# Kernel tuning notes

Measured on AMD Instinct MI355X. Metric: run time of the kernel, lower is better.

The kernel has to match this reference:

```python
import jax, jax.numpy as jnp
import numpy as np

N = 100000
E_ADJ = 800000
E_RAY = 800000
IN_DIM = 2
HID = 64
HEADS = 2
NEG_SLOPE = 0.2  # PyG GATv2Conv default


def setup_inputs() -> dict:
    key = jax.random.key(0)
    ks = jax.random.split(key, 16)
    s = 0.1
    p = lambda k, shape: (jax.random.normal(k, shape, jnp.float32) * s)
    inp = {
        "x": jax.random.normal(ks[0], (N, IN_DIM), jnp.float32),
        "edge_adj": jax.random.randint(ks[1], (2, E_ADJ), 0, N, jnp.int32),
        "edge_ray": jax.random.randint(ks[2], (2, E_RAY), 0, N, jnp.int32),
        # layer 1 params, stacked over the 2 relation types [adjacent, ray]
        "l1_Wl": p(ks[3], (2, IN_DIM, HEADS * HID)),
        "l1_bl": jnp.zeros((2, HEADS * HID), jnp.float32),
        "l1_Wr": p(ks[4], (2, IN_DIM, HEADS * HID)),
        "l1_br": jnp.zeros((2, HEADS * HID), jnp.float32),
        "l1_att": p(ks[5], (2, HEADS, HID)),
        "l1_bias": jnp.zeros((2, HID), jnp.float32),
        # layer 2 params
        "l2_Wl": p(ks[6], (2, HID, HEADS * HID)),
        "l2_bl": jnp.zeros((2, HEADS * HID), jnp.float32),
        "l2_Wr": p(ks[7], (2, HID, HEADS * HID)),
        "l2_br": jnp.zeros((2, HEADS * HID), jnp.float32),
        "l2_att": p(ks[8], (2, HEADS, HID)),
        "l2_bias": jnp.zeros((2, HID), jnp.float32),
    }
    return inp


def _gatv2(x, src, dst, Wl, bl, Wr, br, att, bias):
    # GATv2Conv, concat=False, add_self_loops=False (PyG semantics)
    n = x.shape[0]
    H, C = att.shape
    xl = (x @ Wl + bl).reshape(n, H, C)  # source transform
    xr = (x @ Wr + br).reshape(n, H, C)  # target transform
    e = jax.nn.leaky_relu(xl[src] + xr[dst], NEG_SLOPE)  # [E,H,C]
    score = jnp.einsum('ehc,hc->eh', e, att)             # [E,H]
    # segment softmax over incoming edges per destination (per head)
    m = jax.ops.segment_max(score, dst, num_segments=n)  # only gathered at non-empty segs
    ex = jnp.exp(score - m[dst])
    denom = jax.ops.segment_sum(ex, dst, num_segments=n)
    alpha = ex / (denom[dst] + 1e-16)                    # [E,H]
    out = jax.ops.segment_sum(xl[src] * alpha[:, :, None], dst, num_segments=n)  # [N,H,C]
    return out.mean(axis=1) + bias                       # concat=False -> head mean


def _hetero_layer(x, ea, er, Wl, bl, Wr, br, att, bias):
    o_adj = _gatv2(x, ea[0], ea[1], Wl[0], bl[0], Wr[0], br[0], att[0], bias[0])
    o_ray = _gatv2(x, er[0], er[1], Wl[1], bl[1], Wr[1], br[1], att[1], bias[1])
    return 0.5 * (o_adj + o_ray)  # HeteroConv aggr='mean' over 2 relations


def reference(x, edge_adj, edge_ray,
              l1_Wl, l1_bl, l1_Wr, l1_br, l1_att, l1_bias,
              l2_Wl, l2_bl, l2_Wr, l2_br, l2_att, l2_bias):
    h = _hetero_layer(x, edge_adj, edge_ray, l1_Wl, l1_bl, l1_Wr, l1_br, l1_att, l1_bias)
    h = jax.nn.relu(h)
    out = _hetero_layer(h, edge_adj, edge_ray, l2_Wl, l2_bl, l2_Wr, l2_br, l2_att, l2_bias)
    return out
```

## Files before the change

### kernel.cpp

```cpp
#include <hip/hip_runtime.h>
#include <hip/hip_bf16.h>

typedef __hip_bfloat16 bf16;
typedef unsigned int uint;
typedef unsigned short ushort;
typedef __attribute__((ext_vector_type(8))) short short8;
typedef __attribute__((ext_vector_type(4))) float floatx4;

#define N_NODES 100000
#define N_PAD   100096
#define E_EDGES 800000
#define NBLK    98
#define NSLICE  8
#define SLICE_N 12512
#define SLICE_BLOCKS 512

static __device__ __forceinline__ uint packbf(float a, float b) {
  bf16 x = __float2bfloat16(a), y = __float2bfloat16(b);
  ushort ux = *reinterpret_cast<ushort*>(&x);
  ushort uy = *reinterpret_cast<ushort*>(&y);
  return (uint)ux | ((uint)uy << 16);
}
static __device__ __forceinline__ float lo16(uint u) { return __uint_as_float(u << 16); }
static __device__ __forceinline__ float hi16(uint u) { return __uint_as_float(u & 0xffff0000u); }

__global__ void hist_sliced_k(const int* __restrict__ dst0, const int* __restrict__ dst1,
                              int* dg0, int* dg1) {
  int slice = blockIdx.x & (NSLICE - 1);
  int blk = blockIdx.x >> 3;
  int lo = slice * SLICE_N, hi = lo + SLICE_N;
  for (int i = blk * 256 + threadIdx.x; i < E_EDGES; i += SLICE_BLOCKS * 256) {
    int d0 = __builtin_nontemporal_load(dst0 + i);
    if (d0 >= lo && d0 < hi) atomicAdd(&dg0[d0], 1);
    int d1 = __builtin_nontemporal_load(dst1 + i);
    if (d1 >= lo && d1 < hi) atomicAdd(&dg1[d1], 1);
  }
}

__global__ void scat_sliced_k(const int* __restrict__ src0, const int* __restrict__ dst0,
                              const int* __restrict__ src1, const int* __restrict__ dst1,
                              int* fi0, int* fi1, int2* csd0, int2* csd1) {
  int slice = blockIdx.x & (NSLICE - 1);
  int blk = blockIdx.x >> 3;
  int lo = slice * SLICE_N, hi = lo + SLICE_N;
  for (int i = blk * 256 + threadIdx.x; i < E_EDGES; i += SLICE_BLOCKS * 256) {
    int d0 = __builtin_nontemporal_load(dst0 + i);
    if (d0 >= lo && d0 < hi) {
      int s = __builtin_nontemporal_load(src0 + i);
      int p = atomicAdd(&fi0[d0], 1);
      csd0[p] = make_int2(s, d0);
    }
    int d1 = __builtin_nontemporal_load(dst1 + i);
    if (d1 >= lo && d1 < hi) {
      int s = __builtin_nontemporal_load(src1 + i);
      int p = atomicAdd(&fi1[d1], 1);
      csd1[p] = make_int2(s, d1);
    }
  }
}

__global__ void scan_blk_k(const int* __restrict__ deg0, const int* __restrict__ deg1,
                           int* rp0, int* rp1, int* bsum) {
  __shared__ int s[1024];
  int r = blockIdx.y;
  const int* deg = r ? deg1 : deg0;
  int* rp = r ? rp1 : rp0;
  int i = blockIdx.x * 1024 + threadIdx.x;
  int v = (i < N_NODES) ? deg[i] : 0;
  s[threadIdx.x] = v;
  __syncthreads();
  for (int off = 1; off < 1024; off <<= 1) {
    int t = (threadIdx.x >= off) ? s[threadIdx.x - off] : 0;
    __syncthreads();
    s[threadIdx.x] += t;
    __syncthreads();
  }
  if (i < N_NODES) rp[i] = s[threadIdx.x] - v;
  if (threadIdx.x == 1023) bsum[r * NBLK + blockIdx.x] = s[1023];
}

__global__ void scan_top_k(int* bsum, int* rp0, int* rp1) {
  __shared__ int s[128];
  int r = blockIdx.x;
  int v = (threadIdx.x < NBLK) ? bsum[r * NBLK + threadIdx.x] : 0;
  s[threadIdx.x] = v;
  __syncthreads();
  for (int off = 1; off < 128; off <<= 1) {
    int t = (threadIdx.x >= off) ? s[threadIdx.x - off] : 0;
    __syncthreads();
    s[threadIdx.x] += t;
    __syncthreads();
  }
  if (threadIdx.x < NBLK) bsum[r * NBLK + threadIdx.x] = s[threadIdx.x] - v;
  if (threadIdx.x == 127) (r ? rp1 : rp0)[N_NODES] = s[127];
}

__global__ void scan_add_k(const int* __restrict__ bsum,
                           int* rp0, int* rp1, int* fi0, int* fi1) {
  int r = blockIdx.y;
  int i = blockIdx.x * 1024 + threadIdx.x;
  if (i >= N_NODES) return;
  int* rp = r ? rp1 : rp0;
  int* fi = r ? fi1 : fi0;
  int val = rp[i] + bsum[r * NBLK + blockIdx.x];
  rp[i] = val;
  fi[i] = val;
}

__global__ void wprep_k(const float* __restrict__ Wl, const float* __restrict__ Wr,
                        short* __restrict__ WT,
                        const float* __restrict__ l1Wl, const float* __restrict__ l1bl,
                        const float* __restrict__ l1Wr, const float* __restrict__ l1br,
                        const float* __restrict__ l1att, float* __restrict__ L1C) {
  if (blockIdx.x == 128) {
    int t = threadIdx.x;
    if (t < 20) {
      int rel = t / 10, rem = t % 10, h = rem / 5, v = rem % 5;
      const float* a = l1att + rel * 128 + h * 64;
      float sum = 0.f;
      for (int c = 0; c < 64; ++c) {
        int cc = h * 64 + c;
        float val;
        if (v == 0)      val = l1bl[rel * 128 + cc] + l1br[rel * 128 + cc];
        else if (v == 1) val = l1Wr[rel * 256 + cc];
        else if (v == 2) val = l1Wr[rel * 256 + 128 + cc];
        else if (v == 3) val = l1Wl[rel * 256 + cc];
        else             val = l1Wl[rel * 256 + 128 + cc];
        sum += a[c] * val;
      }
      L1C[t] = sum;
    }
    return;
  }
  int id2 = blockIdx.x * 256 + threadIdx.x;
  int rel = id2 >> 14;
  int id = id2 & 16383;
  int c = id >> 6, k = id & 63;
  const float* W = (c < 128) ? (Wl + rel * 8192) : (Wr + rel * 8192);
  int cc = c & 127;
  bf16 b = __float2bfloat16(W[k * 128 + cc]);
  WT[rel * 16384 + c * 64 + k] = *reinterpret_cast<short*>(&b);
}

__global__ __launch_bounds__(256) void l1score_k(
    const int2* __restrict__ csd0, const int2* __restrict__ csd1,
    const float* __restrict__ x,
    const float* __restrict__ Wl, const float* __restrict__ bl,
    const float* __restrict__ Wr, const float* __restrict__ br,
    const float* __restrict__ att, const float* __restrict__ l1c,
    float4* __restrict__ EX4) {
  __shared__ float sC[32 * 24];
  int rel = blockIdx.y;
  const int2* csd = rel ? csd1 : csd0;
  const float* Wl_r = Wl + rel * 256;
  const float* Wr_r = Wr + rel * 256;
  const float* bl_r = bl + rel * 128;
  const float* br_r = br + rel * 128;
  const float* att_r = att + rel * 128;
  int t = threadIdx.x;
  if (t < 128) {
    int c = t, ch = c >> 2, o = c & 3;
    sC[ch * 24 + 0 + o]  = bl_r[c] + br_r[c];
    sC[ch * 24 + 4 + o]  = Wr_r[c];
    sC[ch * 24 + 8 + o]  = Wr_r[128 + c];
    sC[ch * 24 + 12 + o] = Wl_r[c];
    sC[ch * 24 + 16 + o] = Wl_r[128 + c];
    sC[ch * 24 + 20 + o] = att_r[c];
  }
  const float* C = l1c + rel * 10;
  float q00 = C[0], qv00 = C[1], qv10 = C[2], qw00 = C[3], qw10 = C[4];
  float q01 = C[5], qv01 = C[6], qv11 = C[7], qw01 = C[8], qw11 = C[9];
  __syncthreads();
  int i = blockIdx.x * 256 + t;
  int2 sd = csd[i];
  int s = sd.x, d = sd.y;
  float2 xs = *(const float2*)(x + 2 * s);
  float2 xd = *(const float2*)(x + 2 * d);
  float t0a = 0.f, t0b = 0.f, t1a = 0.f, t1b = 0.f;
#pragma unroll
  for (int ch = 0; ch < 32; ++ch) {
    const float4* cp = (const float4*)(sC + ch * 24);
    float4 bb = cp[0], v0 = cp[1], v1 = cp[2], w0 = cp[3], w1 = cp[4], aa = cp[5];
    float e0 = bb.x + xd.x * v0.x + xd.y * v1.x + xs.x * w0.x + xs.y * w1.x;
    float e1 = bb.y + xd.x * v0.y + xd.y * v1.y + xs.x * w0.y + xs.y * w1.y;
    float e2 = bb.z + xd.x * v0.z + xd.y * v1.z + xs.x * w0.z + xs.y * w1.z;
    float e3 = bb.w + xd.x * v0.w + xd.y * v1.w + xs.x * w0.w + xs.y * w1.w;
    if (ch < 16) {
      t0a = fmaf(aa.x, fabsf(e0), t0a); t0b = fmaf(aa.y, fabsf(e1), t0b);
      t0a = fmaf(aa.z, fabsf(e2), t0a); t0b = fmaf(aa.w, fabsf(e3), t0b);
    } else {
      t1a = fmaf(aa.x, fabsf(e0), t1a); t1b = fmaf(aa.y, fabsf(e1), t1b);
      t1a = fmaf(aa.z, fabsf(e2), t1a); t1b = fmaf(aa.w, fabsf(e3), t1b);
    }
  }
  float T0 = t0a + t0b, T1 = t1a + t1b;
  float lin0 = q00 + xd.x * qv00 + xd.y * qv10 + xs.x * qw00 + xs.y * qw10;
  float lin1 = q01 + xd.x * qv01 + xd.y * qv11 + xs.x * qw01 + xs.y * qw11;
  float p0 = fmaf(0.4f, T0, 0.6f * lin0);
  float p1 = fmaf(0.4f, T1, 0.6f * lin1);
  EX4[(size_t)rel * E_EDGES + i] = make_float4(__expf(p0), __expf(p1), xs.x, xs.y);
}

__global__ __launch_bounds__(256) void l1agg_k(
    const int* __restrict__ rp0, const int* __restrict__ rp1,
    const float4* __restrict__ EX4, float* __restrict__ NA) {
  int g = (blockIdx.x * 256 + threadIdx.x) >> 2;
  int k = threadIdx.x & 3;
  if (g >= N_NODES) return;
  float p0 = 0.f, p1 = 0.f, p2 = 0.f, p3 = 0.f, p4 = 0.f, p5 = 0.f;
  float p6 = 0.f, p7 = 0.f, p8 = 0.f, p9 = 0.f, p10 = 0.f, p11 = 0.f;
  {
    int beg = rp0[g], end = rp0[g + 1];
    for (int j = beg + k; j < end; j += 4) {
      float4 e = EX4[j];
      p0 += e.x; p1 = fmaf(e.x, e.z, p1); p2 = fmaf(e.x, e.w, p2);
      p3 += e.y; p4 = fmaf(e.y, e.z, p4); p5 = fmaf(e.y, e.w, p5);
    }
  }
  {
    const float4* E1 = EX4 + E_EDGES;
    int beg = rp1[g], end = rp1[g + 1];
    for (int j = beg + k; j < end; j += 4) {
      float4 e = E1[j];
      p6 += e.x; p7 = fmaf(e.x, e.z, p7); p8 = fmaf(e.x, e.w, p8);
      p9 += e.y; p10 = fmaf(e.y, e.z, p10); p11 = fmaf(e.y, e.w, p11);
    }
  }
#define RED4(v) v += __shfl_xor(v, 1); v += __shfl_xor(v, 2);
  RED4(p0) RED4(p1) RED4(p2) RED4(p3) RED4(p4) RED4(p5)
  RED4(p6) RED4(p7) RED4(p8) RED4(p9) RED4(p10) RED4(p11)
#undef RED4
  float* na = NA + (size_t)g * 16;
  if (k == 0)      *(float4*)(na)     = make_float4(p0, p1, p2, p3);
  else if (k == 1) *(float4*)(na + 4) = make_float4(p4, p5, p6, p7);
  else if (k == 2) *(float4*)(na + 8) = make_float4(p8, p9, p10, p11);
}

__global__ __launch_bounds__(256) void l1finish_k(
    const float* __restrict__ NA,
    const float* __restrict__ Wl, const float* __restrict__ bl,
    const float* __restrict__ bias, uint2* __restrict__ HB2) {
  int idx = blockIdx.x * 256 + threadIdx.x;
  int d = idx >> 4, l = idx & 15;
  int c0 = 4 * l;
  const float* na = NA + (size_t)d * 16;
  float out0 = 0.f, out1 = 0.f, out2 = 0.f, out3 = 0.f;
#pragma unroll
  for (int r = 0; r < 2; ++r) {
    float a0c = 0.f, a1c = 0.f, a2c = 0.f, a3c = 0.f;
#pragma unroll
    for (int h = 0; h < 2; ++h) {
      float den = na[r * 6 + h * 3 + 0];
      float A0  = na[r * 6 + h * 3 + 1];
      float A1  = na[r * 6 + h * 3 + 2];
      float inv = 1.f / (den + 1e-16f);
      float a0 = A0 * inv, a1 = A1 * inv, S = den * inv;
      float4 W0 = *(const float4*)(Wl + r * 256 + h * 64 + c0);
      float4 W1 = *(const float4*)(Wl + r * 256 + 128 + h * 64 + c0);
      float4 B  = *(const float4*)(bl + r * 128 + h * 64 + c0);
      a0c += a0 * W0.x + a1 * W1.x + S * B.x;
      a1c += a0 * W0.y + a1 * W1.y + S * B.y;
      a2c += a0 * W0.z + a1 * W1.z + S * B.z;
      a3c += a0 * W0.w + a1 * W1.w + S * B.w;
    }
    float4 bi = *(const float4*)(bias + r * 64 + c0);
    out0 += 0.5f * a0c + bi.x;
    out1 += 0.5f * a1c + bi.y;
    out2 += 0.5f * a2c + bi.z;
    out3 += 0.5f * a3c + bi.w;
  }
  out0 = fmaxf(0.5f * out0, 0.f); out1 = fmaxf(0.5f * out1, 0.f);
  out2 = fmaxf(0.5f * out2, 0.f); out3 = fmaxf(0.5f * out3, 0.f);
  HB2[(size_t)d * 16 + l] = make_uint2(packbf(out0, out1), packbf(out2, out3));
}

__global__ __launch_bounds__(256) void mfma_t_k(const bf16* __restrict__ HB,
                                                const short* __restrict__ WTb,
                                                const float* __restrict__ blb,
                                                const float* __restrict__ brb,
                                                bf16* __restrict__ XL0,
                                                bf16* __restrict__ XR0,
                                                bf16* __restrict__ XL1,
                                                bf16* __restrict__ XR1) {
  __shared__ short sW[256 * 72];
  int rel = blockIdx.z;
  const short* WT = WTb + rel * 16384;
  const float* bl = blb + rel * 128;
  const float* br = brb + rel * 128;
  bf16* XLp = rel ? XL1 : XL0;
  bf16* XRp = rel ? XR1 : XR0;
  int t = threadIdx.x;
#pragma unroll
  for (int i = 0; i < 8; ++i) {
    int chunk = t + i * 256;
    int c = chunk >> 3, off = (chunk & 7) * 8;
    *(short8*)(&sW[c * 72 + off]) = *(const short8*)(WT + chunk * 8);
  }
  __syncthreads();
  int wave = t >> 6, lane = t & 63;
  int q = lane >> 4, m = lane & 15;
  int rowbase = blockIdx.x * 128 + wave * 32;
  short8 afr[2][2];
#pragma unroll
  for (int rt = 0; rt < 2; ++rt)
#pragma unroll
    for (int kh = 0; kh < 2; ++kh) {
      size_t row = (size_t)(rowbase + rt * 16 + m);
      afr[rt][kh] = *(const short8*)((const short*)HB + row * 64 + kh * 32 + q * 8);
    }
  for (int ct = 0; ct < 16; ++ct) {
    int col = ct * 16 + m;
    short8 b0 = *(const short8*)(&sW[col * 72 + q * 8]);
    short8 b1 = *(const short8*)(&sW[col * 72 + 32 + q * 8]);
    float bias = (col < 128) ? bl[col] : br[col - 128];
    bf16* X = (col < 128) ? XLp : XRp;
    int c128 = col & 127;
#pragma unroll
    for (int rt = 0; rt < 2; ++rt) {
      floatx4 acc = {0.f, 0.f, 0.f, 0.f};
      acc = __builtin_amdgcn_mfma_f32_16x16x32_bf16(afr[rt][0], b0, acc, 0, 0, 0);
      acc = __builtin_amdgcn_mfma_f32_16x16x32_bf16(afr[rt][1], b1, acc, 0, 0, 0);
      int r0 = rowbase + rt * 16 + q * 4;
#pragma unroll
      for (int i2 = 0; i2 < 4; ++i2) {
        int row = r0 + i2;
        if (row < N_NODES)
          X[(size_t)row * 128 + c128] = __float2bfloat16(acc[i2] + bias);
      }
    }
  }
}

struct EdgeAcc { float a0, a1, a2, a3, den; };

static __device__ __forceinline__ void edge_step(
    uint2 u, float xr0, float xr1, float xr2, float xr3,
    float at0, float at1, float at2, float at3, EdgeAcc& A) {
  float x0 = lo16(u.x), x1 = hi16(u.x), x2 = lo16(u.y), x3 = hi16(u.y);
  float e0 = x0 + xr0; e0 = e0 > 0.f ? e0 : 0.2f * e0;
  float e1 = x1 + xr1; e1 = e1 > 0.f ? e1 : 0.2f * e1;
  float e2 = x2 + xr2; e2 = e2 > 0.f ? e2 : 0.2f * e2;
  float e3 = x3 + xr3; e3 = e3 > 0.f ? e3 : 0.2f * e3;
  float p = e0 * at0 + e1 * at1 + e2 * at2 + e3 * at3;
  p += __shfl_xor(p, 1);
  p += __shfl_xor(p, 2);
  p += __shfl_xor(p, 4);
  p += __shfl_xor(p, 8);
  float ex = __expf(p);
  A.den += ex;
  A.a0 += ex * x0; A.a1 += ex * x1; A.a2 += ex * x2; A.a3 += ex * x3;
}

__global__ __launch_bounds__(256) void aggh_k(
    const int* __restrict__ rp, const int2* __restrict__ csd,
    const bf16* __restrict__ XL, const bf16* __restrict__ XR,
    const float* __restrict__ att, const float* __restrict__ bias,
    float* __restrict__ accum, float* __restrict__ outf, int phase) {
  int d = (blockIdx.x * 256 + threadIdx.x) >> 6;
  int lane = threadIdx.x & 63;
  if (d >= N_NODES) return;
  int half = lane >> 5;
  int l = lane & 31;
  const float* at = att + 4 * l;
  float at0 = at[0], at1 = at[1], at2 = at[2], at3 = at[3];
  uint2 ur = *(const uint2*)(XR + (size_t)d * 128 + 4 * l);
  float xr0 = lo16(ur.x), xr1 = hi16(ur.x), xr2 = lo16(ur.y), xr3 = hi16(ur.y);
  EdgeAcc A = {0.f, 0.f, 0.f, 0.f, 0.f};
  int beg = rp[d], end = rp[d + 1];
  int j = beg + half;
  for (; j + 2 < end; j += 4) {
    int sA = csd[j].x, sB = csd[j + 2].x;
    uint2 uA = *(const uint2*)(XL + (size_t)sA * 128 + 4 * l);
    uint2 uB = *(const uint2*)(XL + (size_t)sB * 128 + 4 * l);
    edge_step(uA, xr0, xr1, xr2, xr3, at0, at1, at2, at3, A);
    edge_step(uB, xr0, xr1, xr2, xr3, at0, at1, at2, at3, A);
  }
  for (; j < end; j += 2) {
    int s = csd[j].x;
    uint2 u = *(const uint2*)(XL + (size_t)s * 128 + 4 * l);
    edge_step(u, xr0, xr1, xr2, xr3, at0, at1, at2, at3, A);
  }
  A.den += __shfl_xor(A.den, 32);
  A.a0 += __shfl_xor(A.a0, 32);
  A.a1 += __shfl_xor(A.a1, 32);
  A.a2 += __shfl_xor(A.a2, 32);
  A.a3 += __shfl_xor(A.a3, 32);
  float inv = 1.f / (A.den + 1e-16f);
  A.a0 *= inv; A.a1 *= inv; A.a2 *= inv; A.a3 *= inv;
  float o0 = 0.5f * (A.a0 + __shfl_xor(A.a0, 16));
  float o1 = 0.5f * (A.a1 + __shfl_xor(A.a1, 16));
  float o2 = 0.5f * (A.a2 + __shfl_xor(A.a2, 16));
  float o3 = 0.5f * (A.a3 + __shfl_xor(A.a3, 16));
  if (lane >= 16) return;
  int c0 = 4 * lane;
  o0 += bias[c0]; o1 += bias[c0 + 1]; o2 += bias[c0 + 2]; o3 += bias[c0 + 3];
  size_t oi = (size_t)d * 64 + c0;
  if (phase == 0) {
    *(float4*)(accum + oi) = make_float4(o0, o1, o2, o3);
  } else {
    float4 pa = *(const float4*)(accum + oi);
    float v0 = 0.5f * (pa.x + o0);
    float v1 = 0.5f * (pa.y + o1);
    float v2 = 0.5f * (pa.z + o2);
    float v3 = 0.5f * (pa.w + o3);
    *(float4*)(outf + oi) = make_float4(v0, v1, v2, v3);
  }
}

extern "C" void kernel_launch(void* const* d_in, const int* in_sizes, int n_in,
                              void* d_out, int out_size, void* d_ws, size_t ws_size,
                              hipStream_t stream) {
  const float* x       = (const float*)d_in[0];
  const int*   e_adj   = (const int*)d_in[1];
  const int*   e_ray   = (const int*)d_in[2];
  const float* l1_Wl   = (const float*)d_in[3];
  const float* l1_bl   = (const float*)d_in[4];
  const float* l1_Wr   = (const float*)d_in[5];
  const float* l1_br   = (const float*)d_in[6];
  const float* l1_att  = (const float*)d_in[7];
  const float* l1_bias = (const float*)d_in[8];
  const float* l2_Wl   = (const float*)d_in[9];
  const float* l2_bl   = (const float*)d_in[10];
  const float* l2_Wr   = (const float*)d_in[11];
  const float* l2_br   = (const float*)d_in[12];
  const float* l2_att  = (const float*)d_in[13];
  const float* l2_bias = (const float*)d_in[14];
  float* out = (float*)d_out;

  char* w = (char*)d_ws;
  size_t off = 0;
  auto alloc = [&](size_t bytes) -> char* {
    char* p = w + off;
    off += (bytes + 255) & ~(size_t)255;
    return p;
  };
  bf16* XL0  = (bf16*)alloc((size_t)N_PAD * 128 * 2);
  bf16* XR0  = (bf16*)alloc((size_t)N_PAD * 128 * 2);
  bf16* XL1  = (bf16*)alloc((size_t)N_PAD * 128 * 2);
  bf16* XR1  = (bf16*)alloc((size_t)N_PAD * 128 * 2);
  bf16* HB   = (bf16*)alloc((size_t)N_PAD * 64 * 2);
  short* WT  = (short*)alloc(2 * 16384 * 2);
  int* RP0   = (int*)alloc((size_t)(N_NODES + 1) * 4);
  int* RP1   = (int*)alloc((size_t)(N_NODES + 1) * 4);
  int* FI0   = (int*)alloc((size_t)N_NODES * 4);
  int* FI1   = (int*)alloc((size_t)N_NODES * 4);
  int2* CSD0 = (int2*)alloc((size_t)E_EDGES * 8);
  int2* CSD1 = (int2*)alloc((size_t)E_EDGES * 8);
  int* DG0   = (int*)alloc((size_t)N_NODES * 4);
  int* DG1   = (int*)alloc((size_t)N_NODES * 4);
  int* BSUM  = (int*)alloc(2 * NBLK * 4);
  float* L1C = (float*)alloc(20 * 4);
  float* ACC = out;

  float4* EX4 = (float4*)XL0;
  float* NA   = (float*)((char*)XL0 + 25600000);

  const int* src_adj = e_adj;
  const int* dst_adj = e_adj + E_EDGES;
  const int* src_ray = e_ray;
  const int* dst_ray = e_ray + E_EDGES;

  const int WNB = (N_NODES * 64) / 256;
  const int MB  = N_PAD / 128;
  const int SB  = SLICE_BLOCKS * NSLICE;

  size_t dgspan = (size_t)((char*)DG1 - (char*)DG0) + (size_t)N_NODES * 4;
  hipMemsetAsync(DG0, 0, dgspan, stream);
  hist_sliced_k<<<SB, 256, 0, stream>>>(dst_adj, dst_ray, DG0, DG1);
  scan_blk_k<<<dim3(NBLK, 2), 1024, 0, stream>>>(DG0, DG1, RP0, RP1, BSUM);
  scan_top_k<<<2, 128, 0, stream>>>(BSUM, RP0, RP1);
  scan_add_k<<<dim3(NBLK, 2), 1024, 0, stream>>>(BSUM, RP0, RP1, FI0, FI1);
  scat_sliced_k<<<SB, 256, 0, stream>>>(src_adj, dst_adj, src_ray, dst_ray,
                                        FI0, FI1, CSD0, CSD1);
  wprep_k<<<129, 256, 0, stream>>>(l2_Wl, l2_Wr, WT,
                                   l1_Wl, l1_bl, l1_Wr, l1_br, l1_att, L1C);

  l1score_k<<<dim3(E_EDGES / 256, 2), 256, 0, stream>>>(
      CSD0, CSD1, x, l1_Wl, l1_bl, l1_Wr, l1_br, l1_att, L1C, EX4);
  l1agg_k<<<(N_NODES * 4 + 255) / 256, 256, 0, stream>>>(RP0, RP1, EX4, NA);
  l1finish_k<<<(N_NODES * 16) / 256, 256, 0, stream>>>(NA, l1_Wl, l1_bl, l1_bias,
                                                       (uint2*)HB);

  mfma_t_k<<<dim3(MB, 1, 2), 256, 0, stream>>>(HB, WT, l2_bl, l2_br,
                                               XL0, XR0, XL1, XR1);
  aggh_k<<<WNB, 256, 0, stream>>>(RP0, CSD0, XL0, XR0, l2_att, l2_bias,
                                  ACC, nullptr, 0);
  aggh_k<<<WNB, 256, 0, stream>>>(RP1, CSD1, XL1, XR1, l2_att + 128, l2_bias + 64,
                                  ACC, out, 1);
}
```

Measured before the change: 492.7 us.

## Partition edges by destination slice once before the CSR histogram and scatter

```diff
diff --git a/kernel.cpp b/kernel.cpp
--- a/kernel.cpp
+++ b/kernel.cpp
@@ -13,7 +13,8 @@
 #define NBLK    98
 #define NSLICE  8
 #define SLICE_N 12512
-#define SLICE_BLOCKS 512
+#define PCAP    384
+#define PBLK    512
 
 static __device__ __forceinline__ uint packbf(float a, float b) {
   bf16 x = __float2bfloat16(a), y = __float2bfloat16(b);
@@ -24,38 +25,119 @@
 static __device__ __forceinline__ float lo16(uint u) { return __uint_as_float(u << 16); }
 static __device__ __forceinline__ float hi16(uint u) { return __uint_as_float(u & 0xffff0000u); }
 
-__global__ void hist_sliced_k(const int* __restrict__ dst0, const int* __restrict__ dst1,
-                              int* dg0, int* dg1) {
-  int slice = blockIdx.x & (NSLICE - 1);
-  int blk = blockIdx.x >> 3;
-  int lo = slice * SLICE_N, hi = lo + SLICE_N;
-  for (int i = blk * 256 + threadIdx.x; i < E_EDGES; i += SLICE_BLOCKS * 256) {
-    int d0 = __builtin_nontemporal_load(dst0 + i);
-    if (d0 >= lo && d0 < hi) atomicAdd(&dg0[d0], 1);
-    int d1 = __builtin_nontemporal_load(dst1 + i);
-    if (d1 >= lo && d1 < hi) atomicAdd(&dg1[d1], 1);
-  }
-}
-
-__global__ void scat_sliced_k(const int* __restrict__ src0, const int* __restrict__ dst0,
-                              const int* __restrict__ src1, const int* __restrict__ dst1,
-                              int* fi0, int* fi1, int2* csd0, int2* csd1) {
-  int slice = blockIdx.x & (NSLICE - 1);
-  int blk = blockIdx.x >> 3;
-  int lo = slice * SLICE_N, hi = lo + SLICE_N;
-  for (int i = blk * 256 + threadIdx.x; i < E_EDGES; i += SLICE_BLOCKS * 256) {
-    int d0 = __builtin_nontemporal_load(dst0 + i);
-    if (d0 >= lo && d0 < hi) {
-      int s = __builtin_nontemporal_load(src0 + i);
-      int p = atomicAdd(&fi0[d0], 1);
-      csd0[p] = make_int2(s, d0);
-    }
-    int d1 = __builtin_nontemporal_load(dst1 + i);
-    if (d1 >= lo && d1 < hi) {
-      int s = __builtin_nontemporal_load(src1 + i);
-      int p = atomicAdd(&fi1[d1], 1);
-      csd1[p] = make_int2(s, d1);
-    }
+__global__ __launch_bounds__(256) void bhist_k(const int* __restrict__ dst0,
+                                               const int* __restrict__ dst1,
+                                               int* __restrict__ bcnt) {
+  __shared__ int h[16];
+  int t = threadIdx.x;
+  if (t < 16) h[t] = 0;
+  __syncthreads();
+  for (int i = blockIdx.x * 256 + t; i < E_EDGES; i += 1024 * 256) {
+    atomicAdd(&h[dst0[i] / SLICE_N], 1);
+    atomicAdd(&h[8 + dst1[i] / SLICE_N], 1);
+  }
+  __syncthreads();
+  if (t < 16 && h[t]) atomicAdd(&bcnt[t], h[t]);
+}
+
+__global__ void bscan_k(const int* __restrict__ bcnt, int* __restrict__ bbase,
+                        int* __restrict__ gtail) {
+  if (threadIdx.x == 0) {
+    for (int r = 0; r < 2; ++r) {
+      int run = 0;
+      for (int b = 0; b < 8; ++b) {
+        int idx = r * 8 + b;
+        bbase[idx] = run;
+        gtail[idx] = run;
+        run += bcnt[idx];
+      }
+    }
+  }
+}
+
+__global__ __launch_bounds__(256) void part_k(
+    const int* __restrict__ src0, const int* __restrict__ dst0,
+    const int* __restrict__ src1, const int* __restrict__ dst1,
+    int* __restrict__ gtail, int2* __restrict__ pb) {
+  __shared__ int2 bins[8][PCAP];
+  __shared__ int cnt[8];
+  __shared__ int sb[8];
+  int rel = blockIdx.y;
+  const int* src = rel ? src1 : src0;
+  const int* dst = rel ? dst1 : dst0;
+  int2* out = pb + (size_t)rel * E_EDGES;
+  int* gt = gtail + rel * 8;
+  int t = threadIdx.x;
+  if (t < 8) cnt[t] = 0;
+  __syncthreads();
+  for (int i0 = blockIdx.x * 256; i0 < E_EDGES; i0 += PBLK * 256) {
+    int i = i0 + t;
+    int d = dst[i], s = src[i];
+    int b = d / SLICE_N;
+    int p = atomicAdd(&cnt[b], 1);
+    bins[b][p] = make_int2(s, d);
+    __syncthreads();
+#pragma unroll
+    for (int b2 = 0; b2 < 8; ++b2) {
+      if (t == 0 && cnt[b2] >= 128) sb[b2] = atomicAdd(&gt[b2], cnt[b2]);
+    }
+    __syncthreads();
+#pragma unroll
+    for (int b2 = 0; b2 < 8; ++b2) {
+      int n = cnt[b2];
+      if (n >= 128) {
+        int gbase = sb[b2];
+        for (int k = t; k < n; k += 256) out[gbase + k] = bins[b2][k];
+      }
+    }
+    __syncthreads();
+    if (t < 8 && cnt[t] >= 128) cnt[t] = 0;
+    __syncthreads();
+  }
+#pragma unroll
+  for (int b2 = 0; b2 < 8; ++b2) {
+    if (t == 0 && cnt[b2] > 0) sb[b2] = atomicAdd(&gt[b2], cnt[b2]);
+  }
+  __syncthreads();
+#pragma unroll
+  for (int b2 = 0; b2 < 8; ++b2) {
+    int n = cnt[b2];
+    if (n > 0) {
+      int gbase = sb[b2];
+      for (int k = t; k < n; k += 256) out[gbase + k] = bins[b2][k];
+    }
+  }
+}
+
+__global__ __launch_bounds__(256) void hist2_k(
+    const int2* __restrict__ pb, const int* __restrict__ bbase,
+    const int* __restrict__ bcnt, int* dg0, int* dg1) {
+  int rel = blockIdx.y;
+  int slice = blockIdx.x & (NSLICE - 1), blk = blockIdx.x >> 3;
+  int idx = rel * 8 + slice;
+  const int2* p = pb + (size_t)rel * E_EDGES + bbase[idx];
+  int n = bcnt[idx];
+  int* dg = rel ? dg1 : dg0;
+  for (int i = blk * 256 + threadIdx.x; i < n; i += 64 * 256) {
+    atomicAdd(&dg[p[i].y], 1);
+  }
+}
+
+__global__ __launch_bounds__(256) void scat2_k(
+    const int2* __restrict__ pb, const int* __restrict__ bbase,
+    const int* __restrict__ bcnt, int* fi0, int* fi1,
+    int2* csd0, int2* csd1) {
+  int rel = blockIdx.y;
+  int slice = blockIdx.x & (NSLICE - 1), blk = blockIdx.x >> 3;
+  int idx = rel * 8 + slice;
+  const int2* p = pb + (size_t)rel * E_EDGES + bbase[idx];
+  int n = bcnt[idx];
+  int* fi = rel ? fi1 : fi0;
+  int2* csd = rel ? csd1 : csd0;
+  for (int i = blk * 256 + threadIdx.x; i < n; i += 64 * 256) {
+    int2 e = p[i];
+    int q = atomicAdd(&fi[e.y], 1);
+    csd[q] = e;
   }
 }
 
@@ -450,10 +532,14 @@
   int* DG1   = (int*)alloc((size_t)N_NODES * 4);
   int* BSUM  = (int*)alloc(2 * NBLK * 4);
   float* L1C = (float*)alloc(20 * 4);
+  int* BCNT  = (int*)alloc(16 * 4);
+  int* BBASE = (int*)alloc(16 * 4);
+  int* GTAIL = (int*)alloc(16 * 4);
   float* ACC = out;
 
   float4* EX4 = (float4*)XL0;
   float* NA   = (float*)((char*)XL0 + 25600000);
+  int2* PB    = (int2*)XL1;
 
   const int* src_adj = e_adj;
   const int* dst_adj = e_adj + E_EDGES;
@@ -462,16 +548,19 @@
 
   const int WNB = (N_NODES * 64) / 256;
   const int MB  = N_PAD / 128;
-  const int SB  = SLICE_BLOCKS * NSLICE;
 
   size_t dgspan = (size_t)((char*)DG1 - (char*)DG0) + (size_t)N_NODES * 4;
   hipMemsetAsync(DG0, 0, dgspan, stream);
-  hist_sliced_k<<<SB, 256, 0, stream>>>(dst_adj, dst_ray, DG0, DG1);
+  hipMemsetAsync(BCNT, 0, 768, stream);
+  bhist_k<<<1024, 256, 0, stream>>>(dst_adj, dst_ray, BCNT);
+  bscan_k<<<1, 64, 0, stream>>>(BCNT, BBASE, GTAIL);
+  part_k<<<dim3(PBLK, 2), 256, 0, stream>>>(src_adj, dst_adj, src_ray, dst_ray,
+                                            GTAIL, PB);
+  hist2_k<<<dim3(512, 2), 256, 0, stream>>>(PB, BBASE, BCNT, DG0, DG1);
   scan_blk_k<<<dim3(NBLK, 2), 1024, 0, stream>>>(DG0, DG1, RP0, RP1, BSUM);
   scan_top_k<<<2, 128, 0, stream>>>(BSUM, RP0, RP1);
   scan_add_k<<<dim3(NBLK, 2), 1024, 0, stream>>>(BSUM, RP0, RP1, FI0, FI1);
-  scat_sliced_k<<<SB, 256, 0, stream>>>(src_adj, dst_adj, src_ray, dst_ray,
-                                        FI0, FI1, CSD0, CSD1);
+  scat2_k<<<dim3(512, 2), 256, 0, stream>>>(PB, BBASE, BCNT, FI0, FI1, CSD0, CSD1);
   wprep_k<<<129, 256, 0, stream>>>(l2_Wl, l2_Wr, WT,
                                    l1_Wl, l1_bl, l1_Wr, l1_br, l1_att, L1C);
 
```

Result: slower. 692.3 us (+40.5%).

## Build CSR with atomic ranks instead of sliced histogram and atomic scatter

Applied to the files above, without the earlier changes.

```diff
diff --git a/kernel.cpp b/kernel.cpp
--- a/kernel.cpp
+++ b/kernel.cpp
@@ -11,9 +11,7 @@
 #define N_PAD   100096
 #define E_EDGES 800000
 #define NBLK    98
-#define NSLICE  8
-#define SLICE_N 12512
-#define SLICE_BLOCKS 512
+#define EBLK    3125
 
 static __device__ __forceinline__ uint packbf(float a, float b) {
   bf16 x = __float2bfloat16(a), y = __float2bfloat16(b);
@@ -24,39 +22,35 @@
 static __device__ __forceinline__ float lo16(uint u) { return __uint_as_float(u << 16); }
 static __device__ __forceinline__ float hi16(uint u) { return __uint_as_float(u & 0xffff0000u); }
 
-__global__ void hist_sliced_k(const int* __restrict__ dst0, const int* __restrict__ dst1,
-                              int* dg0, int* dg1) {
-  int slice = blockIdx.x & (NSLICE - 1);
-  int blk = blockIdx.x >> 3;
-  int lo = slice * SLICE_N, hi = lo + SLICE_N;
-  for (int i = blk * 256 + threadIdx.x; i < E_EDGES; i += SLICE_BLOCKS * 256) {
-    int d0 = __builtin_nontemporal_load(dst0 + i);
-    if (d0 >= lo && d0 < hi) atomicAdd(&dg0[d0], 1);
-    int d1 = __builtin_nontemporal_load(dst1 + i);
-    if (d1 >= lo && d1 < hi) atomicAdd(&dg1[d1], 1);
-  }
-}
-
-__global__ void scat_sliced_k(const int* __restrict__ src0, const int* __restrict__ dst0,
-                              const int* __restrict__ src1, const int* __restrict__ dst1,
-                              int* fi0, int* fi1, int2* csd0, int2* csd1) {
-  int slice = blockIdx.x & (NSLICE - 1);
-  int blk = blockIdx.x >> 3;
-  int lo = slice * SLICE_N, hi = lo + SLICE_N;
-  for (int i = blk * 256 + threadIdx.x; i < E_EDGES; i += SLICE_BLOCKS * 256) {
-    int d0 = __builtin_nontemporal_load(dst0 + i);
-    if (d0 >= lo && d0 < hi) {
-      int s = __builtin_nontemporal_load(src0 + i);
-      int p = atomicAdd(&fi0[d0], 1);
-      csd0[p] = make_int2(s, d0);
-    }
-    int d1 = __builtin_nontemporal_load(dst1 + i);
-    if (d1 >= lo && d1 < hi) {
-      int s = __builtin_nontemporal_load(src1 + i);
-      int p = atomicAdd(&fi1[d1], 1);
-      csd1[p] = make_int2(s, d1);
-    }
-  }
+__global__ __launch_bounds__(256) void rank_k(
+    const int* __restrict__ dst0, const int* __restrict__ dst1,
+    int* fi0, int* fi1, int* __restrict__ rk0, int* __restrict__ rk1) {
+  int i = blockIdx.x * 256 + threadIdx.x;
+  int rel = blockIdx.y;
+  const int* dst = rel ? dst1 : dst0;
+  int* fi = rel ? fi1 : fi0;
+  int* rk = rel ? rk1 : rk0;
+  int d = dst[i];
+  rk[i] = atomicAdd(&fi[d], 1);
+}
+
+__global__ __launch_bounds__(256) void scat_rank_k(
+    const int* __restrict__ src0, const int* __restrict__ dst0,
+    const int* __restrict__ src1, const int* __restrict__ dst1,
+    const int* __restrict__ rk0, const int* __restrict__ rk1,
+    const int* __restrict__ rp0, const int* __restrict__ rp1,
+    int2* __restrict__ csd0, int2* __restrict__ csd1) {
+  int i = blockIdx.x * 256 + threadIdx.x;
+  int rel = blockIdx.y;
+  const int* src = rel ? src1 : src0;
+  const int* dst = rel ? dst1 : dst0;
+  const int* rk = rel ? rk1 : rk0;
+  const int* rp = rel ? rp1 : rp0;
+  int2* csd = rel ? csd1 : csd0;
+  int d = dst[i];
+  int s = src[i];
+  int pos = rp[d] + rk[i];
+  csd[pos] = make_int2(s, d);
 }
 
 __global__ void scan_blk_k(const int* __restrict__ deg0, const int* __restrict__ deg1,
@@ -446,14 +440,14 @@
   int* FI1   = (int*)alloc((size_t)N_NODES * 4);
   int2* CSD0 = (int2*)alloc((size_t)E_EDGES * 8);
   int2* CSD1 = (int2*)alloc((size_t)E_EDGES * 8);
-  int* DG0   = (int*)alloc((size_t)N_NODES * 4);
-  int* DG1   = (int*)alloc((size_t)N_NODES * 4);
   int* BSUM  = (int*)alloc(2 * NBLK * 4);
   float* L1C = (float*)alloc(20 * 4);
   float* ACC = out;
 
   float4* EX4 = (float4*)XL0;
   float* NA   = (float*)((char*)XL0 + 25600000);
+  int* RK0    = (int*)XL1;
+  int* RK1    = (int*)((char*)XL1 + 3200000);
 
   const int* src_adj = e_adj;
   const int* dst_adj = e_adj + E_EDGES;
@@ -462,20 +456,19 @@
 
   const int WNB = (N_NODES * 64) / 256;
   const int MB  = N_PAD / 128;
-  const int SB  = SLICE_BLOCKS * NSLICE;
-
-  size_t dgspan = (size_t)((char*)DG1 - (char*)DG0) + (size_t)N_NODES * 4;
-  hipMemsetAsync(DG0, 0, dgspan, stream);
-  hist_sliced_k<<<SB, 256, 0, stream>>>(dst_adj, dst_ray, DG0, DG1);
-  scan_blk_k<<<dim3(NBLK, 2), 1024, 0, stream>>>(DG0, DG1, RP0, RP1, BSUM);
+
+  size_t fispan = (size_t)((char*)FI1 - (char*)FI0) + (size_t)N_NODES * 4;
+  hipMemsetAsync(FI0, 0, fispan, stream);
+  rank_k<<<dim3(EBLK, 2), 256, 0, stream>>>(dst_adj, dst_ray, FI0, FI1, RK0, RK1);
+  scan_blk_k<<<dim3(NBLK, 2), 1024, 0, stream>>>(FI0, FI1, RP0, RP1, BSUM);
   scan_top_k<<<2, 128, 0, stream>>>(BSUM, RP0, RP1);
   scan_add_k<<<dim3(NBLK, 2), 1024, 0, stream>>>(BSUM, RP0, RP1, FI0, FI1);
-  scat_sliced_k<<<SB, 256, 0, stream>>>(src_adj, dst_adj, src_ray, dst_ray,
-                                        FI0, FI1, CSD0, CSD1);
+  scat_rank_k<<<dim3(EBLK, 2), 256, 0, stream>>>(src_adj, dst_adj, src_ray, dst_ray,
+                                                 RK0, RK1, RP0, RP1, CSD0, CSD1);
   wprep_k<<<129, 256, 0, stream>>>(l2_Wl, l2_Wr, WT,
                                    l1_Wl, l1_bl, l1_Wr, l1_br, l1_att, L1C);
 
-  l1score_k<<<dim3(E_EDGES / 256, 2), 256, 0, stream>>>(
+  l1score_k<<<dim3(EBLK, 2), 256, 0, stream>>>(
       CSD0, CSD1, x, l1_Wl, l1_bl, l1_Wr, l1_br, l1_att, L1C, EX4);
   l1agg_k<<<(N_NODES * 4 + 255) / 256, 256, 0, stream>>>(RP0, RP1, EX4, NA);
   l1finish_k<<<(N_NODES * 16) / 256, 256, 0, stream>>>(NA, l1_Wl, l1_bl, l1_bias,
```

Result: faster. 440.6 us (-10.6%).
